# Optimization experiments

Hardware: AMD Instinct MI355X
Metric: run time of the kernel (lower is better)

The kernel has to match this reference:

```python
import jax, jax.numpy as jnp
import numpy as np

DIM = 768
HEADS = 12
HEAD_DIM = DIM // HEADS
HIDDEN = int(DIM * 2.0)
EPS = 1e-5


def layer_norm(x, g, b):
    mu = jnp.mean(x, axis=-1, keepdims=True)
    var = jnp.var(x, axis=-1, keepdims=True)
    return (x - mu) * jax.lax.rsqrt(var + EPS) * g + b


def setup_inputs() -> dict:
    key = jax.random.key(0)
    ks = jax.random.split(key, 10)
    B, N = 8, 1024
    s = 0.02
    return {
        "x": jax.random.normal(ks[0], (B, N, DIM), jnp.float32),
        "rpe_bias": jax.random.normal(ks[1], (HEADS, N, N), jnp.float32),
        # weights stored as (in, out); equals torch Linear weight transposed
        "qkv_w": jax.random.normal(ks[2], (DIM, 3 * DIM), jnp.float32) * s,
        "proj_w": jax.random.normal(ks[3], (DIM, DIM), jnp.float32) * s,
        "proj_b": jnp.zeros((DIM,), jnp.float32),
        "ln1_g": jnp.ones((DIM,), jnp.float32),
        "ln1_b": jnp.zeros((DIM,), jnp.float32),
        "ln2_g": jnp.ones((DIM,), jnp.float32),
        "ln2_b": jnp.zeros((DIM,), jnp.float32),
        "fc1_w": jax.random.normal(ks[4], (DIM, HIDDEN), jnp.float32) * s,
        "fc1_b": jnp.zeros((HIDDEN,), jnp.float32),
        "fc2_w": jax.random.normal(ks[5], (HIDDEN, DIM), jnp.float32) * s,
        "fc2_b": jnp.zeros((DIM,), jnp.float32),
    }


def reference(x, rpe_bias, qkv_w, proj_w, proj_b, ln1_g, ln1_b, ln2_g, ln2_b,
              fc1_w, fc1_b, fc2_w, fc2_b):
    B, N, C = x.shape
    scale = HEAD_DIM ** -0.5

    # ---- attention branch (pre-norm) ----
    h = layer_norm(x, ln1_g, ln1_b)
    qkv = h @ qkv_w                                   # [B,N,3C]
    qkv = qkv.reshape(B, N, 3, HEADS, HEAD_DIM)
    q = jnp.transpose(qkv[:, :, 0], (0, 2, 1, 3))     # [B,H,N,D]
    k = jnp.transpose(qkv[:, :, 1], (0, 2, 1, 3))
    v = jnp.transpose(qkv[:, :, 2], (0, 2, 1, 3))
    attn = jnp.einsum('bhnd,bhmd->bhnm', q, k) * scale + rpe_bias[None]
    attn = jax.nn.softmax(attn, axis=-1)
    o = jnp.einsum('bhnm,bhmd->bhnd', attn, v)        # [B,H,N,D]
    o = jnp.transpose(o, (0, 2, 1, 3)).reshape(B, N, C)
    x = x + (o @ proj_w + proj_b)

    # ---- MLP branch (pre-norm) ----
    h = layer_norm(x, ln2_g, ln2_b)
    h = jax.nn.gelu(h @ fc1_w + fc1_b, approximate=False)
    x = x + (h @ fc2_w + fc2_b)
    return x
```

## Files before the change

### kernel.cpp

```cpp
#include <hip/hip_runtime.h>

typedef __bf16 bf16;
typedef __bf16 bf16x8 __attribute__((ext_vector_type(8)));
typedef float f32x4 __attribute__((ext_vector_type(4)));

#define DIM 768
#define HEADS 12
#define HD 64
#define HIDDEN 1536
#define BB 8
#define NN 1024
#define ROWS (BB*NN)

__device__ __forceinline__ void gload_lds16(const void* g, void* l) {
  __builtin_amdgcn_global_load_lds(
      (const __attribute__((address_space(1))) void*)g,
      (__attribute__((address_space(3))) void*)l, 16, 0, 0);
}

__global__ __launch_bounds__(256) void rpe_cvt_kernel(
    const float* __restrict__ in, bf16* __restrict__ out)
{
  const size_t total = (size_t)HEADS * NN * NN;
  const size_t stride = (size_t)gridDim.x * 256 * 4;
  for (size_t i = ((size_t)blockIdx.x * 256 + threadIdx.x) * 4; i < total; i += stride) {
    const float4 v = *(const float4*)(in + i);
    ushort4 u;
    u.x = __builtin_bit_cast(unsigned short, (bf16)v.x);
    u.y = __builtin_bit_cast(unsigned short, (bf16)v.y);
    u.z = __builtin_bit_cast(unsigned short, (bf16)v.z);
    u.w = __builtin_bit_cast(unsigned short, (bf16)v.w);
    *(ushort4*)(out + i) = u;
  }
}

__global__ __launch_bounds__(256) void ln_kernel(
    const float* __restrict__ x, const float* __restrict__ gw,
    const float* __restrict__ bw, bf16* __restrict__ out)
{
  const int row = blockIdx.x;
  const int tid = threadIdx.x;
  const float* xr = x + (size_t)row * DIM;
  float v0 = xr[tid], v1 = xr[tid + 256], v2 = xr[tid + 512];
  float s1 = v0 + v1 + v2;
  float s2 = v0*v0 + v1*v1 + v2*v2;
#pragma unroll
  for (int off = 1; off < 64; off <<= 1) {
    s1 += __shfl_xor(s1, off);
    s2 += __shfl_xor(s2, off);
  }
  __shared__ float red[8];
  const int w = tid >> 6, lane = tid & 63;
  if (lane == 0) { red[w] = s1; red[4 + w] = s2; }
  __syncthreads();
  s1 = red[0] + red[1] + red[2] + red[3];
  s2 = red[4] + red[5] + red[6] + red[7];
  const float mu = s1 * (1.f / DIM);
  const float rstd = rsqrtf(s2 * (1.f / DIM) - mu * mu + 1e-5f);
  bf16* orow = out + (size_t)row * DIM;
  orow[tid]       = (bf16)((v0 - mu) * rstd * gw[tid]       + bw[tid]);
  orow[tid + 256] = (bf16)((v1 - mu) * rstd * gw[tid + 256] + bw[tid + 256]);
  orow[tid + 512] = (bf16)((v2 - mu) * rstd * gw[tid + 512] + bw[tid + 512]);
}

__global__ void wtrans_kernel(const float* __restrict__ in, bf16* __restrict__ out,
                              int K, int N)
{
  __shared__ float t[32][33];
  const int tx = threadIdx.x, ty = threadIdx.y;
  const int n0 = blockIdx.x * 32, k0 = blockIdx.y * 32;
#pragma unroll
  for (int i = 0; i < 32; i += 8)
    t[ty + i][tx] = in[(size_t)(k0 + ty + i) * N + n0 + tx];
  __syncthreads();
#pragma unroll
  for (int i = 0; i < 32; i += 8)
    out[(size_t)(n0 + ty + i) * K + k0 + tx] = (bf16)t[tx][ty + i];
}

template<int EPI>
__global__ __launch_bounds__(256, 2) void gemm128(
    const bf16* __restrict__ A, const bf16* __restrict__ Bt,
    int M, int N, int K,
    const float* __restrict__ bias, const float* __restrict__ resid,
    void* __restrict__ o0, void* __restrict__ o1, void* __restrict__ o2)
{
  __shared__ bf16 sA[128 * 64];
  __shared__ bf16 sB[128 * 64];
  const int tid = threadIdx.x;
  const int lane = tid & 63, w = tid >> 6;
  const int wrow = w >> 1, wcol = w & 1;
  const int m0 = blockIdx.y * 128, n0 = blockIdx.x * 128;
  const int l15 = lane & 15, l4 = lane >> 4;

  f32x4 acc[4][4] = {};

  const int crow = lane >> 3;
  const int cbyte = (lane & 7) * 16;
  const int ksteps = K >> 6;
  for (int kt = 0; kt < ksteps; ++kt) {
    const int k0 = kt << 6;
    __syncthreads();
#pragma unroll
    for (int c2 = 0; c2 < 4; ++c2) {
      const int c = (w << 2) + c2;
      const int r = (c << 3) + crow;
      gload_lds16((const char*)(A + (size_t)(m0 + r) * K + k0) + cbyte,
                  (char*)sA + c * 1024);
      gload_lds16((const char*)(Bt + (size_t)(n0 + r) * K + k0) + cbyte,
                  (char*)sB + c * 1024);
    }
    __syncthreads();
#pragma unroll
    for (int kk = 0; kk < 64; kk += 32) {
      bf16x8 af[4], bfv[4];
#pragma unroll
      for (int mf = 0; mf < 4; ++mf)
        af[mf] = *(const bf16x8*)(sA + (wrow * 64 + mf * 16 + l15) * 64 + kk + l4 * 8);
#pragma unroll
      for (int nf = 0; nf < 4; ++nf)
        bfv[nf] = *(const bf16x8*)(sB + (wcol * 64 + nf * 16 + l15) * 64 + kk + l4 * 8);
#pragma unroll
      for (int mf = 0; mf < 4; ++mf)
#pragma unroll
        for (int nf = 0; nf < 4; ++nf)
          acc[mf][nf] = __builtin_amdgcn_mfma_f32_16x16x32_bf16(af[mf], bfv[nf], acc[mf][nf], 0, 0, 0);
    }
  }

#pragma unroll
  for (int mf = 0; mf < 4; ++mf) {
    const int rbase = m0 + wrow * 64 + mf * 16 + l4 * 4;
#pragma unroll
    for (int nf = 0; nf < 4; ++nf) {
      const int colbase = n0 + wcol * 64 + nf * 16;
      const int col = colbase + l15;
      if constexpr (EPI == 0) {
        const int seg = colbase / 768;
        const int hh_ = (colbase - seg * 768) >> 6;
        const int dd = (colbase & 63) + l15;
        const int b_ = rbase >> 10;
        const int ns = rbase & 1023;
        const size_t gh = (size_t)(b_ * HEADS + hh_);
        bf16* Qb = (bf16*)o0; bf16* Kb = (bf16*)o1; bf16* Vtb = (bf16*)o2;
        if (seg == 0) {
#pragma unroll
          for (int rg = 0; rg < 4; ++rg)
            Qb[(gh * NN + ns + rg) * HD + dd] = (bf16)(acc[mf][nf][rg] * 0.125f);
        } else if (seg == 1) {
#pragma unroll
          for (int rg = 0; rg < 4; ++rg)
            Kb[(gh * NN + ns + rg) * HD + dd] = (bf16)acc[mf][nf][rg];
        } else {
          union { ushort4 u4; unsigned short us[4]; } pk;
#pragma unroll
          for (int rg = 0; rg < 4; ++rg)
            pk.us[rg] = __builtin_bit_cast(unsigned short, (bf16)acc[mf][nf][rg]);
          *(ushort4*)(Vtb + (gh * HD + dd) * NN + ns) = pk.u4;
        }
      } else if constexpr (EPI == 1 || EPI == 3) {
        float* outp = (float*)o0;
#pragma unroll
        for (int rg = 0; rg < 4; ++rg) {
          const size_t idx = (size_t)(rbase + rg) * N + col;
          outp[idx] = acc[mf][nf][rg] + bias[col] + resid[idx];
        }
      } else {
        bf16* outp = (bf16*)o0;
#pragma unroll
        for (int rg = 0; rg < 4; ++rg) {
          float v = acc[mf][nf][rg] + bias[col];
          float gl = 0.5f * v * (1.0f + erff(v * 0.70710678118654752f));
          outp[(size_t)(rbase + rg) * N + col] = (bf16)gl;
        }
      }
    }
  }
}

__global__ __launch_bounds__(256, 4) void attn_kernel(
    const bf16* __restrict__ Qb, const bf16* __restrict__ Kb,
    const bf16* __restrict__ Vtb, const bf16* __restrict__ rpeb,
    bf16* __restrict__ o_attn)
{
  __shared__ bf16 sK[2][64 * 64];
  __shared__ bf16 sV[2][64 * 64];
  __shared__ bf16 sP[4 * 16 * 64];
  const int tid = threadIdx.x;
  const int lane = tid & 63, w = tid >> 6;
  const int l15 = lane & 15, l4 = lane >> 4;
  const int bid = blockIdx.x;
  const int g = bid >> 4, qt = bid & 15;
  const int b_ = g / HEADS, h_ = g % HEADS;
  const int qbase = qt * 64 + w * 16;

  bf16x8 qf[2];
  {
    const bf16* qp = Qb + ((size_t)g * NN + qbase + l15) * HD + l4 * 8;
    qf[0] = *(const bf16x8*)qp;
    qf[1] = *(const bf16x8*)(qp + 32);
  }

  f32x4 oacc[4] = {};
  float m_r[4] = {-1e30f, -1e30f, -1e30f, -1e30f};
  float l_r[4] = {};
  const bf16* rpe_h = rpeb + (size_t)h_ * NN * NN;

  const int crow = lane >> 3;
  const int scol = ((lane & 7) * 16) ^ ((crow & 7) << 4);
  const int cc = w * 2;

#define STAGE(buf, kv0s) do {                                                      \
    _Pragma("unroll")                                                              \
    for (int c2 = 0; c2 < 2; ++c2) {                                               \
      const int c = cc + c2;                                                       \
      const int r = c * 8 + crow;                                                  \
      gload_lds16((const char*)(Kb + ((size_t)g * NN + (kv0s)) * HD) + r * 128 + scol, \
                  (char*)sK[buf] + c * 1024);                                      \
      gload_lds16((const char*)(Vtb + ((size_t)g * HD + r) * NN + (kv0s)) + scol,  \
                  (char*)sV[buf] + c * 1024);                                      \
    } } while (0)

  STAGE(0, 0);
  __syncthreads();
  int cur = 0;

  for (int kv0 = 0; kv0 < NN; kv0 += 64) {
    if (kv0 + 64 < NN) STAGE(cur ^ 1, kv0 + 64);

    float rv[4][4];
#pragma unroll
    for (int nf = 0; nf < 4; ++nf)
#pragma unroll
      for (int rg = 0; rg < 4; ++rg)
        rv[nf][rg] = (float)rpe_h[(size_t)(qbase + l4 * 4 + rg) * NN + kv0 + nf * 16 + l15];

    f32x4 s[4] = {};
#pragma unroll
    for (int kh = 0; kh < 2; ++kh) {
#pragma unroll
      for (int nf = 0; nf < 4; ++nf) {
        const int n_ = nf * 16 + l15;
        const bf16x8 kf = *(const bf16x8*)((const char*)sK[cur] + n_ * 128 +
                            (((kh * 32 + l4 * 8) * 2) ^ ((n_ & 7) << 4)));
        s[nf] = __builtin_amdgcn_mfma_f32_16x16x32_bf16(qf[kh], kf, s[nf], 0, 0, 0);
      }
    }
    float rm[4] = {-1e30f, -1e30f, -1e30f, -1e30f};
#pragma unroll
    for (int nf = 0; nf < 4; ++nf)
#pragma unroll
      for (int rg = 0; rg < 4; ++rg) {
        float v = s[nf][rg] + rv[nf][rg];
        s[nf][rg] = v;
        rm[rg] = fmaxf(rm[rg], v);
      }
#pragma unroll
    for (int off = 1; off <= 8; off <<= 1)
#pragma unroll
      for (int rg = 0; rg < 4; ++rg)
        rm[rg] = fmaxf(rm[rg], __shfl_xor(rm[rg], off));
    float al[4];
#pragma unroll
    for (int rg = 0; rg < 4; ++rg) {
      const float mn = fmaxf(m_r[rg], rm[rg]);
      al[rg] = __expf(m_r[rg] - mn);
      m_r[rg] = mn;
    }
    float rs[4] = {};
#pragma unroll
    for (int nf = 0; nf < 4; ++nf)
#pragma unroll
      for (int rg = 0; rg < 4; ++rg) {
        const float p = __expf(s[nf][rg] - m_r[rg]);
        rs[rg] += p;
        const int r = l4 * 4 + rg;
        const int cb = (nf * 16 + l15) * 2;
        *(bf16*)((char*)sP + w * 2048 + r * 128 + (cb ^ ((r & 7) << 4))) = (bf16)p;
      }
#pragma unroll
    for (int off = 1; off <= 8; off <<= 1)
#pragma unroll
      for (int rg = 0; rg < 4; ++rg)
        rs[rg] += __shfl_xor(rs[rg], off);
#pragma unroll
    for (int rg = 0; rg < 4; ++rg)
      l_r[rg] = l_r[rg] * al[rg] + rs[rg];
#pragma unroll
    for (int df = 0; df < 4; ++df)
#pragma unroll
      for (int rg = 0; rg < 4; ++rg)
        oacc[df][rg] *= al[rg];

#pragma unroll
    for (int kh = 0; kh < 2; ++kh) {
      const bf16x8 pf = *(const bf16x8*)((const char*)sP + w * 2048 + l15 * 128 +
                          (((kh * 32 + l4 * 8) * 2) ^ ((l15 & 7) << 4)));
#pragma unroll
      for (int df = 0; df < 4; ++df) {
        const int d_ = df * 16 + l15;
        const bf16x8 vf = *(const bf16x8*)((const char*)sV[cur] + d_ * 128 +
                            (((kh * 32 + l4 * 8) * 2) ^ ((d_ & 7) << 4)));
        oacc[df] = __builtin_amdgcn_mfma_f32_16x16x32_bf16(pf, vf, oacc[df], 0, 0, 0);
      }
    }
    __syncthreads();
    cur ^= 1;
  }
#undef STAGE

#pragma unroll
  for (int rg = 0; rg < 4; ++rg) {
    const float inv = 1.0f / l_r[rg];
    const int qr = qbase + l4 * 4 + rg;
    bf16* orow = o_attn + ((size_t)(b_ * NN) + qr) * DIM + h_ * HD;
#pragma unroll
    for (int df = 0; df < 4; ++df)
      orow[df * 16 + l15] = (bf16)(oacc[df][rg] * inv);
  }
}

extern "C" void kernel_launch(void* const* d_in, const int* in_sizes, int n_in,
                              void* d_out, int out_size, void* d_ws, size_t ws_size,
                              hipStream_t stream)
{
  const float* x      = (const float*)d_in[0];
  const float* rpe    = (const float*)d_in[1];
  const float* qkv_w  = (const float*)d_in[2];
  const float* proj_w = (const float*)d_in[3];
  const float* proj_b = (const float*)d_in[4];
  const float* ln1_g  = (const float*)d_in[5];
  const float* ln1_b  = (const float*)d_in[6];
  const float* ln2_g  = (const float*)d_in[7];
  const float* ln2_b  = (const float*)d_in[8];
  const float* fc1_w  = (const float*)d_in[9];
  const float* fc1_b  = (const float*)d_in[10];
  const float* fc2_w  = (const float*)d_in[11];
  const float* fc2_b  = (const float*)d_in[12];
  float* out = (float*)d_out;

  char* ws = (char*)d_ws;
  size_t off = 0;
  bf16* qkv_wT  = (bf16*)(ws + off); off += (size_t)2304 * 768 * 2;
  bf16* proj_wT = (bf16*)(ws + off); off += (size_t)768 * 768 * 2;
  bf16* fc1_wT  = (bf16*)(ws + off); off += (size_t)1536 * 768 * 2;
  bf16* fc2_wT  = (bf16*)(ws + off); off += (size_t)768 * 1536 * 2;
  bf16* hbuf    = (bf16*)(ws + off); off += (size_t)ROWS * DIM * 2;
  bf16* Qb      = (bf16*)(ws + off); off += (size_t)96 * NN * HD * 2;
  bf16* Kb      = (bf16*)(ws + off); off += (size_t)96 * NN * HD * 2;
  bf16* Vtb     = (bf16*)(ws + off); off += (size_t)96 * HD * NN * 2;
  float* x1     = (float*)(ws + off); off += (size_t)ROWS * DIM * 4;
  bf16* o_attn = hbuf;
  bf16* h2 = Qb;
  bf16* hh = Kb;
  bf16* rpeb = (bf16*)x1;

  dim3 tb(32, 8);
  wtrans_kernel<<<dim3(2304 / 32, 768 / 32), tb, 0, stream>>>(qkv_w, qkv_wT, 768, 2304);
  wtrans_kernel<<<dim3(768 / 32, 768 / 32),  tb, 0, stream>>>(proj_w, proj_wT, 768, 768);
  wtrans_kernel<<<dim3(1536 / 32, 768 / 32), tb, 0, stream>>>(fc1_w, fc1_wT, 768, 1536);
  wtrans_kernel<<<dim3(768 / 32, 1536 / 32), tb, 0, stream>>>(fc2_w, fc2_wT, 1536, 768);
  rpe_cvt_kernel<<<3072, 256, 0, stream>>>(rpe, rpeb);

  ln_kernel<<<ROWS, 256, 0, stream>>>(x, ln1_g, ln1_b, hbuf);
  gemm128<0><<<dim3(2304 / 128, ROWS / 128), 256, 0, stream>>>(
      hbuf, qkv_wT, ROWS, 2304, 768, nullptr, nullptr, (void*)Qb, (void*)Kb, (void*)Vtb);
  attn_kernel<<<96 * 16, 256, 0, stream>>>(Qb, Kb, Vtb, rpeb, o_attn);
  gemm128<1><<<dim3(768 / 128, ROWS / 128), 256, 0, stream>>>(
      o_attn, proj_wT, ROWS, 768, 768, proj_b, x, (void*)x1, nullptr, nullptr);
  ln_kernel<<<ROWS, 256, 0, stream>>>(x1, ln2_g, ln2_b, h2);
  gemm128<2><<<dim3(1536 / 128, ROWS / 128), 256, 0, stream>>>(
      h2, fc1_wT, ROWS, 1536, 768, fc1_b, nullptr, (void*)hh, nullptr, nullptr);
  gemm128<3><<<dim3(768 / 128, ROWS / 128), 256, 0, stream>>>(
      hh, fc2_wT, ROWS, 768, 1536, fc2_b, x1, (void*)out, nullptr, nullptr);
}
```

Before: 399.3 us.

## Double-buffer GEMM tiles, add MFMA priority hints, and lazily rescale attention

The GEMM kernel now uses two LDS buffers so the next K-tile's global-to-LDS load is issued before computing on the current one, dropping one barrier per iteration. The attention kernel wraps its MFMA sections in s_setprio to favour matrix issue. It also skips the online-softmax rescale of the accumulators unless some row's max has grown by more than a threshold. Double buffering doubles GEMM LDS use, which may hurt occupancy under launch_bounds(256,2). The lazy rescale trades exactness of the running max for fewer exp and multiply operations and relies on the threshold keeping exp values bounded.

```diff
diff --git a/kernel.cpp b/kernel.cpp
--- a/kernel.cpp
+++ b/kernel.cpp
@@ -85,8 +85,8 @@
     const float* __restrict__ bias, const float* __restrict__ resid,
     void* __restrict__ o0, void* __restrict__ o1, void* __restrict__ o2)
 {
-  __shared__ bf16 sA[128 * 64];
-  __shared__ bf16 sB[128 * 64];
+  __shared__ bf16 sA[2][128 * 64];
+  __shared__ bf16 sB[2][128 * 64];
   const int tid = threadIdx.x;
   const int lane = tid & 63, w = tid >> 6;
   const int wrow = w >> 1, wcol = w & 1;
@@ -98,35 +98,42 @@
   const int crow = lane >> 3;
   const int cbyte = (lane & 7) * 16;
   const int ksteps = K >> 6;
+
+#define STAGE_G(bufg, k0s) do {                                                \
+    _Pragma("unroll")                                                          \
+    for (int c2 = 0; c2 < 4; ++c2) {                                           \
+      const int c = (w << 2) + c2;                                             \
+      const int r = (c << 3) + crow;                                           \
+      gload_lds16((const char*)(A + (size_t)(m0 + r) * K + (k0s)) + cbyte,     \
+                  (char*)sA[bufg] + c * 1024);                                 \
+      gload_lds16((const char*)(Bt + (size_t)(n0 + r) * K + (k0s)) + cbyte,    \
+                  (char*)sB[bufg] + c * 1024);                                 \
+    } } while (0)
+
+  STAGE_G(0, 0);
+  __syncthreads();
+  int cur = 0;
   for (int kt = 0; kt < ksteps; ++kt) {
-    const int k0 = kt << 6;
-    __syncthreads();
-#pragma unroll
-    for (int c2 = 0; c2 < 4; ++c2) {
-      const int c = (w << 2) + c2;
-      const int r = (c << 3) + crow;
-      gload_lds16((const char*)(A + (size_t)(m0 + r) * K + k0) + cbyte,
-                  (char*)sA + c * 1024);
-      gload_lds16((const char*)(Bt + (size_t)(n0 + r) * K + k0) + cbyte,
-                  (char*)sB + c * 1024);
-    }
-    __syncthreads();
+    if (kt + 1 < ksteps) STAGE_G(cur ^ 1, (kt + 1) << 6);
 #pragma unroll
     for (int kk = 0; kk < 64; kk += 32) {
       bf16x8 af[4], bfv[4];
 #pragma unroll
       for (int mf = 0; mf < 4; ++mf)
-        af[mf] = *(const bf16x8*)(sA + (wrow * 64 + mf * 16 + l15) * 64 + kk + l4 * 8);
+        af[mf] = *(const bf16x8*)(sA[cur] + (wrow * 64 + mf * 16 + l15) * 64 + kk + l4 * 8);
 #pragma unroll
       for (int nf = 0; nf < 4; ++nf)
-        bfv[nf] = *(const bf16x8*)(sB + (wcol * 64 + nf * 16 + l15) * 64 + kk + l4 * 8);
+        bfv[nf] = *(const bf16x8*)(sB[cur] + (wcol * 64 + nf * 16 + l15) * 64 + kk + l4 * 8);
 #pragma unroll
       for (int mf = 0; mf < 4; ++mf)
 #pragma unroll
         for (int nf = 0; nf < 4; ++nf)
           acc[mf][nf] = __builtin_amdgcn_mfma_f32_16x16x32_bf16(af[mf], bfv[nf], acc[mf][nf], 0, 0, 0);
     }
-  }
+    __syncthreads();
+    cur ^= 1;
+  }
+#undef STAGE_G
 
 #pragma unroll
   for (int mf = 0; mf < 4; ++mf) {
@@ -236,6 +243,7 @@
         rv[nf][rg] = (float)rpe_h[(size_t)(qbase + l4 * 4 + rg) * NN + kv0 + nf * 16 + l15];
 
     f32x4 s[4] = {};
+    __builtin_amdgcn_s_setprio(1);
 #pragma unroll
     for (int kh = 0; kh < 2; ++kh) {
 #pragma unroll
@@ -246,6 +254,7 @@
         s[nf] = __builtin_amdgcn_mfma_f32_16x16x32_bf16(qf[kh], kf, s[nf], 0, 0, 0);
       }
     }
+    __builtin_amdgcn_s_setprio(0);
     float rm[4] = {-1e30f, -1e30f, -1e30f, -1e30f};
 #pragma unroll
     for (int nf = 0; nf < 4; ++nf)
@@ -260,12 +269,21 @@
 #pragma unroll
       for (int rg = 0; rg < 4; ++rg)
         rm[rg] = fmaxf(rm[rg], __shfl_xor(rm[rg], off));
-    float al[4];
-#pragma unroll
-    for (int rg = 0; rg < 4; ++rg) {
-      const float mn = fmaxf(m_r[rg], rm[rg]);
-      al[rg] = __expf(m_r[rg] - mn);
-      m_r[rg] = mn;
+
+    float mneed = rm[0] - m_r[0];
+#pragma unroll
+    for (int rg = 1; rg < 4; ++rg) mneed = fmaxf(mneed, rm[rg] - m_r[rg]);
+    if (!__all(mneed <= 8.0f)) {
+#pragma unroll
+      for (int rg = 0; rg < 4; ++rg) {
+        const float mn = fmaxf(m_r[rg], rm[rg]);
+        const float al = __expf(m_r[rg] - mn);
+        m_r[rg] = mn;
+        l_r[rg] *= al;
+#pragma unroll
+        for (int df = 0; df < 4; ++df)
+          oacc[df][rg] *= al;
+      }
     }
     float rs[4] = {};
 #pragma unroll
@@ -285,13 +303,9 @@
         rs[rg] += __shfl_xor(rs[rg], off);
 #pragma unroll
     for (int rg = 0; rg < 4; ++rg)
-      l_r[rg] = l_r[rg] * al[rg] + rs[rg];
-#pragma unroll
-    for (int df = 0; df < 4; ++df)
-#pragma unroll
-      for (int rg = 0; rg < 4; ++rg)
-        oacc[df][rg] *= al[rg];
-
+      l_r[rg] += rs[rg];
+
+    __builtin_amdgcn_s_setprio(1);
 #pragma unroll
     for (int kh = 0; kh < 2; ++kh) {
       const bf16x8 pf = *(const bf16x8*)((const char*)sP + w * 2048 + l15 * 128 +
@@ -304,6 +318,7 @@
         oacc[df] = __builtin_amdgcn_mfma_f32_16x16x32_bf16(pf, vf, oacc[df], 0, 0, 0);
       }
     }
+    __builtin_amdgcn_s_setprio(0);
     __syncthreads();
     cur ^= 1;
   }
```

Measured after the change: 431.2 us. 1.08x slower.
